# Optimization experiments

Measured on AMD Instinct MI355X. Metric: run time of the kernel, lower is better.

Reference implementation:

```python
import math
import jax, jax.numpy as jnp
import numpy as np

EMBED_DIM = 1024
N_HEADS = 16
HEAD_DIM = EMBED_DIM // N_HEADS
B, T = 4, 2048


def setup_inputs() -> dict:
    key = jax.random.key(0)
    k1, k2, k3 = jax.random.split(key, 3)
    scale_in = 1.0 / math.sqrt(EMBED_DIM)
    return {
        "x": jax.random.normal(k1, (B, T, EMBED_DIM), dtype=jnp.float32),
        "direction": 0,  # 0=FORWARD (causal), 1=RETRODICTION (anti-causal), 2=CORRECTION (causal)
        "qkv_w": jax.random.normal(k2, (EMBED_DIM, 3 * EMBED_DIM), dtype=jnp.float32) * scale_in,
        "qkv_b": jnp.zeros((3 * EMBED_DIM,), dtype=jnp.float32),
        "proj_w": jax.random.normal(k3, (EMBED_DIM, EMBED_DIM), dtype=jnp.float32) * scale_in,
        "proj_b": jnp.zeros((EMBED_DIM,), dtype=jnp.float32),
    }


def reference(x, direction, qkv_w, qkv_b, proj_w, proj_b):
    Bx, Tx, C = x.shape
    qkv = x @ qkv_w + qkv_b                        # [B,T,3C]
    q, k, v = jnp.split(qkv, 3, axis=-1)
    # [B,T,C] -> [B,H,T,D]
    def heads(t):
        return t.reshape(Bx, Tx, N_HEADS, HEAD_DIM).transpose(0, 2, 1, 3)
    q, k, v = heads(q), heads(k), heads(v)
    scale = 1.0 / math.sqrt(HEAD_DIM)
    attn = jnp.einsum('bhqd,bhkd->bhqk', q, k) * scale
    rows = jnp.arange(Tx)[:, None]
    cols = jnp.arange(Tx)[None, :]
    if direction == 1:  # RETRODICTION -> anti-causal (upper triangular allowed)
        mask = cols >= rows
    else:               # FORWARD / CORRECTION -> causal
        mask = cols <= rows
    attn = jnp.where(mask[None, None], attn, -jnp.inf)
    attn = jax.nn.softmax(attn, axis=-1)  # dropout p=0 -> identity
    out = jnp.einsum('bhqk,bhkd->bhqd', attn, v)   # [B,H,T,D]
    out = out.transpose(0, 2, 1, 3).reshape(Bx, Tx, C)
    return out @ proj_w + proj_b
```

## Files before the change

kernel.cpp:

```cpp
#include <hip/hip_runtime.h>
#include <math.h>

typedef __bf16 bf16_t;
typedef bf16_t bf16x8 __attribute__((ext_vector_type(8)));
typedef bf16_t bf16x4 __attribute__((ext_vector_type(4)));
typedef float  f32x4  __attribute__((ext_vector_type(4)));
typedef float  floatv4 __attribute__((ext_vector_type(4)));

#define AS1 __attribute__((address_space(1)))
#define AS3 __attribute__((address_space(3)))

static __device__ __forceinline__ void gld_lds16(const void* g, void* l) {
  __builtin_amdgcn_global_load_lds((const AS1 unsigned int*)g,
                                   (AS3 unsigned int*)l, 16, 0, 0);
}
static __device__ __forceinline__ void block_sync() {
  asm volatile("" ::: "memory");
  __builtin_amdgcn_s_barrier();
  asm volatile("" ::: "memory");
}

__global__ __launch_bounds__(256) void k_cast(const float* __restrict__ in,
                                              bf16_t* __restrict__ out, int n4) {
  int i = blockIdx.x * 256 + threadIdx.x;
  if (i >= n4) return;
  floatv4 v = ((const floatv4*)in)[i];
  bf16x4 o;
  o.x = (bf16_t)v.x; o.y = (bf16_t)v.y; o.z = (bf16_t)v.z; o.w = (bf16_t)v.w;
  ((bf16x4*)out)[i] = o;
}

__global__ __launch_bounds__(256) void k_transpose_cast(const float* __restrict__ in,
                                                        bf16_t* __restrict__ out,
                                                        int R, int Cc) {
  __shared__ float tile[32][33];
  int c0 = blockIdx.x * 32, r0 = blockIdx.y * 32;
  int tx = threadIdx.x, ty = threadIdx.y;
#pragma unroll
  for (int i = 0; i < 32; i += 8)
    tile[ty + i][tx] = in[(size_t)(r0 + ty + i) * Cc + c0 + tx];
  __syncthreads();
#pragma unroll
  for (int i = 0; i < 32; i += 8)
    out[(size_t)(c0 + ty + i) * R + r0 + tx] = (bf16_t)tile[tx][ty + i];
}

__global__ __launch_bounds__(256) void k_gemm_qkv(
    const bf16_t* __restrict__ A, const bf16_t* __restrict__ Bt,
    const float* __restrict__ bias,
    bf16_t* __restrict__ qo, bf16_t* __restrict__ ko, bf16_t* __restrict__ vto) {
  const int K = 1024;
  __shared__ bf16_t As[128 * 32];
  __shared__ bf16_t Bs[128 * 32];
  const int m0 = blockIdx.x * 128, n0 = blockIdx.y * 128;
  const int t = threadIdx.x, lane = t & 63, w = t >> 6;
  const int wr = w >> 1, wc = w & 1;
  const int ln15 = lane & 15, lhi = lane >> 4;

  f32x4 acc[4][4];
#pragma unroll
  for (int m = 0; m < 4; ++m)
#pragma unroll
    for (int n = 0; n < 4; ++n) acc[m][n] = (f32x4){0.f, 0.f, 0.f, 0.f};

  const int sr = t >> 2, sc = (t & 3) * 8;
  const bf16_t* Ab = A + (size_t)(m0 + sr) * K + sc;
  const bf16_t* Bb = Bt + (size_t)(n0 + sr) * K + sc;
  char* AsDst = (char*)As + t * 16;
  char* BsDst = (char*)Bs + t * 16;

  for (int k0 = 0; k0 < K; k0 += 32) {
    gld_lds16(Ab + k0, AsDst);
    gld_lds16(Ab + 64 * K + k0, AsDst + 4096);
    gld_lds16(Bb + k0, BsDst);
    gld_lds16(Bb + 64 * K + k0, BsDst + 4096);
    __syncthreads();
    bf16x8 af[4], bfr[4];
#pragma unroll
    for (int m = 0; m < 4; ++m)
      af[m] = *(const bf16x8*)&As[(wr * 64 + m * 16 + ln15) * 32 + lhi * 8];
#pragma unroll
    for (int n = 0; n < 4; ++n)
      bfr[n] = *(const bf16x8*)&Bs[(wc * 64 + n * 16 + ln15) * 32 + lhi * 8];
#pragma unroll
    for (int m = 0; m < 4; ++m)
#pragma unroll
      for (int n = 0; n < 4; ++n)
        acc[m][n] = __builtin_amdgcn_mfma_f32_16x16x32_bf16(af[m], bfr[n], acc[m][n], 0, 0, 0);
    __syncthreads();
  }
#pragma unroll
  for (int n = 0; n < 4; ++n) {
    int col = n0 + wc * 64 + n * 16 + ln15;
    float bv = bias[col];
    int which = col >> 10;
    int cc = col & 1023;
    int h = cc >> 6, d = cc & 63;
#pragma unroll
    for (int m = 0; m < 4; ++m)
#pragma unroll
      for (int j = 0; j < 4; ++j) {
        int row = m0 + wr * 64 + m * 16 + lhi * 4 + j;
        int b = row >> 11, tt = row & 2047;
        float o = acc[m][n][j] + bv;
        if (which == 0) o *= 0.18033688011112042f;
        bf16_t ob = (bf16_t)o;
        size_t bh = (size_t)(b * 16 + h);
        if (which == 0)      qo[(bh * 2048 + tt) * 64 + d] = ob;
        else if (which == 1) ko[(bh * 2048 + tt) * 64 + d] = ob;
        else                 vto[(bh * 64 + d) * 2048 + tt] = ob;
      }
  }
}

__global__ __launch_bounds__(256) void k_attn3(
    const bf16_t* __restrict__ q, const bf16_t* __restrict__ k,
    const bf16_t* __restrict__ vt, const int* __restrict__ dirp,
    bf16_t* __restrict__ a2) {
  const int T = 2048;
  __shared__ __align__(16) bf16_t smem[16384];
  const int bh = blockIdx.x, b = bh >> 4, h = bh & 15;
  const int jb = blockIdx.y;
  const int t = threadIdx.x, lane = t & 63, w = t >> 6;
  const int ln15 = lane & 15, lhi = lane >> 4;
  const bool anti = (*dirp == 1);

  const bf16_t* kbase = k + (size_t)bh * T * 64;
  const bf16_t* vbase = vt + (size_t)bh * 64 * T;

  auto stage = [&](int kc0, int buf) {
    char* Kd = (char*)smem + buf * 16384;
    char* Vd = Kd + 8192;
#pragma unroll
    for (int s = 0; s < 2; ++s) {
      const int qk = s * 4 + (t >> 6);
      const int krow = kc0 + (qk >> 2) * 32 + ((qk >> 1) & 1) * 4 +
                       ((lane & 15) >> 2) * 8 + (lane & 3);
      const int kcolb = (lane >> 4) * 16 + (qk & 1) * 64;
      gld_lds16((const char*)kbase + (size_t)krow * 128 + kcolb,
                Kd + s * 4096 + t * 16);
      const int gv = qk;
      const int vd = (gv & 3) * 16 + (lane & 15);
      gld_lds16((const char*)vbase + (size_t)vd * 4096 + (size_t)kc0 * 2 +
                    (gv >> 2) * 64 + (lane >> 4) * 16,
                Vd + s * 4096 + t * 16);
    }
  };

#pragma unroll 1
  for (int sel = 0; sel < 2; ++sel) {
    const int qt = sel ? (31 - jb) : jb;
    const int q0 = qt * 64 + w * 16;
    const int qrow = q0 + ln15;

    const bf16_t* qp = q + ((size_t)bh * T + qrow) * 64 + lhi * 8;
    bf16x8 qf0 = *(const bf16x8*)qp;
    bf16x8 qf1 = *(const bf16x8*)(qp + 32);

    f32x4 acc[4];
#pragma unroll
    for (int g = 0; g < 4; ++g) acc[g] = (f32x4){0.f, 0.f, 0.f, 0.f};
    float mrun = -3.0e38f, lrun = 0.f;

    const int kt0 = anti ? qt : 0;
    const int nb = anti ? (32 - qt) : (qt + 1);

    stage(kt0 * 64, 0);
#pragma unroll 1
    for (int i = 0; i < nb; ++i) {
      const int kt = kt0 + i;
      const int buf = i & 1;
      if (i + 1 < nb) {
        stage((kt + 1) * 64, buf ^ 1);
        asm volatile("s_waitcnt vmcnt(4)" ::: "memory");
      } else {
        asm volatile("s_waitcnt vmcnt(0)" ::: "memory");
      }
      block_sync();
      const bf16_t* Kb = smem + buf * 8192;
      const bf16_t* Vb = Kb + 4096;

      float sc[16];
#pragma unroll
      for (int kh = 0; kh < 2; ++kh) {
        bf16x8 k0 = *(const bf16x8*)(Kb + (kh * 4 + 0) * 512 + lane * 8);
        bf16x8 k1 = *(const bf16x8*)(Kb + (kh * 4 + 1) * 512 + lane * 8);
        bf16x8 k2 = *(const bf16x8*)(Kb + (kh * 4 + 2) * 512 + lane * 8);
        bf16x8 k3 = *(const bf16x8*)(Kb + (kh * 4 + 3) * 512 + lane * 8);
        const f32x4 zz = (f32x4){0.f, 0.f, 0.f, 0.f};
        f32x4 slo = __builtin_amdgcn_mfma_f32_16x16x32_bf16(k0, qf0, zz, 0, 0, 0);
        slo = __builtin_amdgcn_mfma_f32_16x16x32_bf16(k1, qf1, slo, 0, 0, 0);
        f32x4 shi = __builtin_amdgcn_mfma_f32_16x16x32_bf16(k2, qf0, zz, 0, 0, 0);
        shi = __builtin_amdgcn_mfma_f32_16x16x32_bf16(k3, qf1, shi, 0, 0, 0);
#pragma unroll
        for (int j = 0; j < 4; ++j) {
          sc[kh * 8 + j] = slo[j];
          sc[kh * 8 + 4 + j] = shi[j];
        }
      }
      if (kt == qt) {
#pragma unroll
        for (int e = 0; e < 16; ++e) {
          const int col = kt * 64 + (e >> 3) * 32 + lhi * 8 + (e & 7);
          const bool ok = anti ? (col >= qrow) : (col <= qrow);
          sc[e] = ok ? sc[e] : -3.0e38f;
        }
      }
      float lmax = sc[0];
#pragma unroll
      for (int e = 1; e < 16; ++e) lmax = fmaxf(lmax, sc[e]);
      if (!__all(lmax <= mrun + 8.f)) {
        float vm = lmax;
        vm = fmaxf(vm, __shfl_xor(vm, 16));
        vm = fmaxf(vm, __shfl_xor(vm, 32));
        const float mn = fmaxf(mrun, vm);
        const float al = __builtin_amdgcn_exp2f(mrun - mn);
        lrun *= al;
#pragma unroll
        for (int g = 0; g < 4; ++g) acc[g] *= al;
        mrun = mn;
      }
      bf16x8 pb0, pb1;
      float rs = 0.f;
#pragma unroll
      for (int e = 0; e < 8; ++e) {
        float p = __builtin_amdgcn_exp2f(sc[e] - mrun);
        rs += p; pb0[e] = (bf16_t)p;
      }
#pragma unroll
      for (int e = 0; e < 8; ++e) {
        float p = __builtin_amdgcn_exp2f(sc[8 + e] - mrun);
        rs += p; pb1[e] = (bf16_t)p;
      }
      lrun += rs;
#pragma unroll
      for (int dg = 0; dg < 4; ++dg) {
        bf16x8 v0 = *(const bf16x8*)(Vb + dg * 512 + lane * 8);
        acc[dg] = __builtin_amdgcn_mfma_f32_16x16x32_bf16(v0, pb0, acc[dg], 0, 0, 0);
      }
#pragma unroll
      for (int dg = 0; dg < 4; ++dg) {
        bf16x8 v1 = *(const bf16x8*)(Vb + (4 + dg) * 512 + lane * 8);
        acc[dg] = __builtin_amdgcn_mfma_f32_16x16x32_bf16(v1, pb1, acc[dg], 0, 0, 0);
      }
      block_sync();
    }

    lrun += __shfl_xor(lrun, 16);
    lrun += __shfl_xor(lrun, 32);
    const float inv = __builtin_amdgcn_rcpf(lrun);
    bf16_t* op = a2 + ((size_t)b * T + qrow) * 1024 + h * 64 + lhi * 4;
#pragma unroll
    for (int g = 0; g < 4; ++g) {
      bf16x4 o4;
#pragma unroll
      for (int jx = 0; jx < 4; ++jx) o4[jx] = (bf16_t)(acc[g][jx] * inv);
      *(bf16x4*)(op + g * 16) = o4;
    }
  }
}

__global__ __launch_bounds__(256) void k_gemm_proj(
    const bf16_t* __restrict__ A, const bf16_t* __restrict__ Bt,
    const float* __restrict__ bias, float* __restrict__ out) {
  const int K = 1024;
  __shared__ bf16_t As[128 * 32];
  __shared__ bf16_t Bs[128 * 32];
  const int m0 = blockIdx.x * 128, n0 = blockIdx.y * 128;
  const int t = threadIdx.x, lane = t & 63, w = t >> 6;
  const int wr = w >> 1, wc = w & 1;
  const int ln15 = lane & 15, lhi = lane >> 4;

  f32x4 acc[4][4];
#pragma unroll
  for (int m = 0; m < 4; ++m)
#pragma unroll
    for (int n = 0; n < 4; ++n) acc[m][n] = (f32x4){0.f, 0.f, 0.f, 0.f};

  const int sr = t >> 2, sc = (t & 3) * 8;
  const bf16_t* Ab = A + (size_t)(m0 + sr) * K + sc;
  const bf16_t* Bb = Bt + (size_t)(n0 + sr) * K + sc;
  char* AsDst = (char*)As + t * 16;
  char* BsDst = (char*)Bs + t * 16;

  for (int k0 = 0; k0 < K; k0 += 32) {
    gld_lds16(Ab + k0, AsDst);
    gld_lds16(Ab + 64 * K + k0, AsDst + 4096);
    gld_lds16(Bb + k0, BsDst);
    gld_lds16(Bb + 64 * K + k0, BsDst + 4096);
    __syncthreads();
    bf16x8 af[4], bfr[4];
#pragma unroll
    for (int m = 0; m < 4; ++m)
      af[m] = *(const bf16x8*)&As[(wr * 64 + m * 16 + ln15) * 32 + lhi * 8];
#pragma unroll
    for (int n = 0; n < 4; ++n)
      bfr[n] = *(const bf16x8*)&Bs[(wc * 64 + n * 16 + ln15) * 32 + lhi * 8];
#pragma unroll
    for (int m = 0; m < 4; ++m)
#pragma unroll
      for (int n = 0; n < 4; ++n)
        acc[m][n] = __builtin_amdgcn_mfma_f32_16x16x32_bf16(af[m], bfr[n], acc[m][n], 0, 0, 0);
    __syncthreads();
  }
#pragma unroll
  for (int n = 0; n < 4; ++n) {
    int col = n0 + wc * 64 + n * 16 + ln15;
    float bv = bias[col];
#pragma unroll
    for (int m = 0; m < 4; ++m)
#pragma unroll
      for (int j = 0; j < 4; ++j) {
        int row = m0 + wr * 64 + m * 16 + lhi * 4 + j;
        out[(size_t)row * 1024 + col] = acc[m][n][j] + bv;
      }
  }
}

extern "C" void kernel_launch(void* const* d_in, const int* in_sizes, int n_in,
                              void* d_out, int out_size, void* d_ws, size_t ws_size,
                              hipStream_t stream) {
  (void)in_sizes; (void)n_in; (void)out_size; (void)ws_size;
  const float* x      = (const float*)d_in[0];
  const int*   dirp   = (const int*)d_in[1];
  const float* qkv_w  = (const float*)d_in[2];
  const float* qkv_b  = (const float*)d_in[3];
  const float* proj_w = (const float*)d_in[4];
  const float* proj_b = (const float*)d_in[5];
  float* out = (float*)d_out;

  char* ws = (char*)d_ws;
  bf16_t* xb   = (bf16_t*)(ws);
  bf16_t* wq_t = (bf16_t*)(ws + 16777216);
  bf16_t* wp_t = (bf16_t*)(ws + 23068672);
  bf16_t* qb   = (bf16_t*)(ws + 25165824);
  bf16_t* kb   = (bf16_t*)(ws + 41943040);
  bf16_t* vtb  = (bf16_t*)(ws + 58720256);
  bf16_t* a2   = xb;

  k_cast<<<8192, 256, 0, stream>>>(x, xb, 2097152);
  k_transpose_cast<<<dim3(96, 32), dim3(32, 8), 0, stream>>>(qkv_w, wq_t, 1024, 3072);
  k_transpose_cast<<<dim3(32, 32), dim3(32, 8), 0, stream>>>(proj_w, wp_t, 1024, 1024);
  k_gemm_qkv<<<dim3(64, 24), 256, 0, stream>>>(xb, wq_t, qkv_b, qb, kb, vtb);
  k_attn3<<<dim3(64, 16), 256, 0, stream>>>(qb, kb, vtb, dirp, a2);
  k_gemm_proj<<<dim3(64, 8), 256, 0, stream>>>(a2, wp_t, proj_b, out);
}
```

Measured before the change: 198.6 us.

## Double-buffer GEMM LDS staging and coalesce QKV epilogue via shared memory

Both GEMM kernels now double-buffer their LDS tiles, issuing the next k-slice's global-to-LDS loads before the MFMAs on the current slice, which leaves one barrier per iteration instead of two. The staging layout is rearranged so each wave loads a 16x32 MFMA fragment contiguously, making fragment reads linear per lane. The QKV epilogue writes the tile into LDS, transposed for V, then stores 16-byte vectors to q/k/vT instead of scattered 2-byte stores. LDS use roughly doubles (about 33 KB per block), which may reduce occupancy.

```diff
diff --git a/kernel.cpp b/kernel.cpp
--- a/kernel.cpp
+++ b/kernel.cpp
@@ -50,8 +50,7 @@
     const float* __restrict__ bias,
     bf16_t* __restrict__ qo, bf16_t* __restrict__ ko, bf16_t* __restrict__ vto) {
   const int K = 1024;
-  __shared__ bf16_t As[128 * 32];
-  __shared__ bf16_t Bs[128 * 32];
+  __shared__ __align__(16) char smem[33792];
   const int m0 = blockIdx.x * 128, n0 = blockIdx.y * 128;
   const int t = threadIdx.x, lane = t & 63, w = t >> 6;
   const int wr = w >> 1, wc = w & 1;
@@ -63,53 +62,84 @@
 #pragma unroll
     for (int n = 0; n < 4; ++n) acc[m][n] = (f32x4){0.f, 0.f, 0.f, 0.f};
 
-  const int sr = t >> 2, sc = (t & 3) * 8;
-  const bf16_t* Ab = A + (size_t)(m0 + sr) * K + sc;
-  const bf16_t* Bb = Bt + (size_t)(n0 + sr) * K + sc;
-  char* AsDst = (char*)As + t * 16;
-  char* BsDst = (char*)Bs + t * 16;
-
-  for (int k0 = 0; k0 < K; k0 += 32) {
-    gld_lds16(Ab + k0, AsDst);
-    gld_lds16(Ab + 64 * K + k0, AsDst + 4096);
-    gld_lds16(Bb + k0, BsDst);
-    gld_lds16(Bb + 64 * K + k0, BsDst + 4096);
-    __syncthreads();
+  const bf16_t* aSrc = A + (size_t)(m0 + w * 16 + ln15) * K + lhi * 8;
+  const bf16_t* bSrc = Bt + (size_t)(n0 + w * 16 + ln15) * K + lhi * 8;
+  char* dstA = smem + t * 16;
+
+  auto stageG = [&](int k0, int buf) {
+    char* base = dstA + buf * 16384;
+    gld_lds16(aSrc + k0, base);
+    gld_lds16(aSrc + 64 * K + k0, base + 4096);
+    gld_lds16(bSrc + k0, base + 8192);
+    gld_lds16(bSrc + 64 * K + k0, base + 12288);
+  };
+
+  stageG(0, 0);
+  asm volatile("s_waitcnt vmcnt(0)" ::: "memory");
+  block_sync();
+  int buf = 0;
+#pragma unroll 2
+  for (int it = 0; it < 32; ++it) {
+    if (it + 1 < 32) stageG((it + 1) * 32, buf ^ 1);
+    const bf16_t* Asb = (const bf16_t*)(smem + buf * 16384);
+    const bf16_t* Bsb = (const bf16_t*)(smem + buf * 16384 + 8192);
     bf16x8 af[4], bfr[4];
 #pragma unroll
     for (int m = 0; m < 4; ++m)
-      af[m] = *(const bf16x8*)&As[(wr * 64 + m * 16 + ln15) * 32 + lhi * 8];
+      af[m] = *(const bf16x8*)(Asb + (wr * 4 + m) * 512 + lane * 8);
 #pragma unroll
     for (int n = 0; n < 4; ++n)
-      bfr[n] = *(const bf16x8*)&Bs[(wc * 64 + n * 16 + ln15) * 32 + lhi * 8];
+      bfr[n] = *(const bf16x8*)(Bsb + (wc * 4 + n) * 512 + lane * 8);
 #pragma unroll
     for (int m = 0; m < 4; ++m)
 #pragma unroll
       for (int n = 0; n < 4; ++n)
         acc[m][n] = __builtin_amdgcn_mfma_f32_16x16x32_bf16(af[m], bfr[n], acc[m][n], 0, 0, 0);
-    __syncthreads();
-  }
+    asm volatile("s_waitcnt vmcnt(0)" ::: "memory");
+    block_sync();
+    buf ^= 1;
+  }
+
+  bf16_t* L = (bf16_t*)smem;
+  const int which = n0 >> 10;
+  const float bscale = (which == 0) ? 0.18033688011112042f : 1.0f;
 #pragma unroll
   for (int n = 0; n < 4; ++n) {
-    int col = n0 + wc * 64 + n * 16 + ln15;
-    float bv = bias[col];
-    int which = col >> 10;
-    int cc = col & 1023;
-    int h = cc >> 6, d = cc & 63;
+    const int col = wc * 64 + n * 16 + ln15;
+    const float bv = bias[n0 + col];
 #pragma unroll
     for (int m = 0; m < 4; ++m)
 #pragma unroll
       for (int j = 0; j < 4; ++j) {
-        int row = m0 + wr * 64 + m * 16 + lhi * 4 + j;
-        int b = row >> 11, tt = row & 2047;
-        float o = acc[m][n][j] + bv;
-        if (which == 0) o *= 0.18033688011112042f;
-        bf16_t ob = (bf16_t)o;
-        size_t bh = (size_t)(b * 16 + h);
-        if (which == 0)      qo[(bh * 2048 + tt) * 64 + d] = ob;
-        else if (which == 1) ko[(bh * 2048 + tt) * 64 + d] = ob;
-        else                 vto[(bh * 64 + d) * 2048 + tt] = ob;
-      }
+        const int row = wr * 64 + m * 16 + lhi * 4 + j;
+        const bf16_t ob = (bf16_t)((acc[m][n][j] + bv) * bscale);
+        if (which == 2) L[col * 132 + row] = ob;
+        else            L[row * 132 + col] = ob;
+      }
+  }
+  block_sync();
+  const int bq = m0 >> 11, ttb = m0 & 2047;
+  if (which == 2) {
+#pragma unroll
+    for (int c = 0; c < 8; ++c) {
+      const int idx = c * 256 + t;
+      const int vcol = idx >> 4, r8 = (idx & 15) * 8;
+      bf16x8 v8 = *(const bf16x8*)&L[vcol * 132 + r8];
+      const int cc = (n0 + vcol) & 1023;
+      const int hh = cc >> 6, d = cc & 63;
+      *(bf16x8*)&vto[((size_t)(bq * 16 + hh) * 64 + d) * 2048 + ttb + r8] = v8;
+    }
+  } else {
+    bf16_t* dst = (which == 0) ? qo : ko;
+#pragma unroll
+    for (int c = 0; c < 8; ++c) {
+      const int idx = c * 256 + t;
+      const int row = idx >> 4, c8 = (idx & 15) * 8;
+      bf16x8 v8 = *(const bf16x8*)&L[row * 132 + c8];
+      const int cc = (n0 & 1023) + c8;
+      const int hh = cc >> 6, d = cc & 63;
+      *(bf16x8*)&dst[((size_t)(bq * 16 + hh) * 2048 + ttb + row) * 64 + d] = v8;
+    }
   }
 }
 
@@ -264,8 +294,7 @@
     const bf16_t* __restrict__ A, const bf16_t* __restrict__ Bt,
     const float* __restrict__ bias, float* __restrict__ out) {
   const int K = 1024;
-  __shared__ bf16_t As[128 * 32];
-  __shared__ bf16_t Bs[128 * 32];
+  __shared__ __align__(16) char smem[32768];
   const int m0 = blockIdx.x * 128, n0 = blockIdx.y * 128;
   const int t = threadIdx.x, lane = t & 63, w = t >> 6;
   const int wr = w >> 1, wc = w & 1;
@@ -277,41 +306,52 @@
 #pragma unroll
     for (int n = 0; n < 4; ++n) acc[m][n] = (f32x4){0.f, 0.f, 0.f, 0.f};
 
-  const int sr = t >> 2, sc = (t & 3) * 8;
-  const bf16_t* Ab = A + (size_t)(m0 + sr) * K + sc;
-  const bf16_t* Bb = Bt + (size_t)(n0 + sr) * K + sc;
-  char* AsDst = (char*)As + t * 16;
-  char* BsDst = (char*)Bs + t * 16;
-
-  for (int k0 = 0; k0 < K; k0 += 32) {
-    gld_lds16(Ab + k0, AsDst);
-    gld_lds16(Ab + 64 * K + k0, AsDst + 4096);
-    gld_lds16(Bb + k0, BsDst);
-    gld_lds16(Bb + 64 * K + k0, BsDst + 4096);
-    __syncthreads();
+  const bf16_t* aSrc = A + (size_t)(m0 + w * 16 + ln15) * K + lhi * 8;
+  const bf16_t* bSrc = Bt + (size_t)(n0 + w * 16 + ln15) * K + lhi * 8;
+  char* dstA = smem + t * 16;
+
+  auto stageG = [&](int k0, int buf) {
+    char* base = dstA + buf * 16384;
+    gld_lds16(aSrc + k0, base);
+    gld_lds16(aSrc + 64 * K + k0, base + 4096);
+    gld_lds16(bSrc + k0, base + 8192);
+    gld_lds16(bSrc + 64 * K + k0, base + 12288);
+  };
+
+  stageG(0, 0);
+  asm volatile("s_waitcnt vmcnt(0)" ::: "memory");
+  block_sync();
+  int buf = 0;
+#pragma unroll 2
+  for (int it = 0; it < 32; ++it) {
+    if (it + 1 < 32) stageG((it + 1) * 32, buf ^ 1);
+    const bf16_t* Asb = (const bf16_t*)(smem + buf * 16384);
+    const bf16_t* Bsb = (const bf16_t*)(smem + buf * 16384 + 8192);
     bf16x8 af[4], bfr[4];
 #pragma unroll
     for (int m = 0; m < 4; ++m)
-      af[m] = *(const bf16x8*)&As[(wr * 64 + m * 16 + ln15) * 32 + lhi * 8];
+      af[m] = *(const bf16x8*)(Asb + (wr * 4 + m) * 512 + lane * 8);
 #pragma unroll
     for (int n = 0; n < 4; ++n)
-      bfr[n] = *(const bf16x8*)&Bs[(wc * 64 + n * 16 + ln15) * 32 + lhi * 8];
+      bfr[n] = *(const bf16x8*)(Bsb + (wc * 4 + n) * 512 + lane * 8);
 #pragma unroll
     for (int m = 0; m < 4; ++m)
 #pragma unroll
       for (int n = 0; n < 4; ++n)
         acc[m][n] = __builtin_amdgcn_mfma_f32_16x16x32_bf16(af[m], bfr[n], acc[m][n], 0, 0, 0);
-    __syncthreads();
+    asm volatile("s_waitcnt vmcnt(0)" ::: "memory");
+    block_sync();
+    buf ^= 1;
   }
 #pragma unroll
   for (int n = 0; n < 4; ++n) {
-    int col = n0 + wc * 64 + n * 16 + ln15;
-    float bv = bias[col];
+    const int col = n0 + wc * 64 + n * 16 + ln15;
+    const float bv = bias[col];
 #pragma unroll
     for (int m = 0; m < 4; ++m)
 #pragma unroll
       for (int j = 0; j < 4; ++j) {
-        int row = m0 + wr * 64 + m * 16 + lhi * 4 + j;
+        const int row = m0 + wr * 64 + m * 16 + lhi * 4 + j;
         out[(size_t)row * 1024 + col] = acc[m][n][j] + bv;
       }
   }
```

New measurement: 223.5 us. 12.5% more time.
